# Performance work log

Hardware: AMD Instinct MI355X
Metric: run time of the kernel (lower is better)

Reference implementation:

```python
import jax, jax.numpy as jnp
import numpy as np

B, T, HID = 1, 2048, 1024
H, D = 16, 64
S = 64            # selection_block_size / sliding window / compress block
MAXK = 8          # max_selected_blocks
W_ENT, W_SP = 0.01, 0.01
NB = T // S       # 32 blocks (T divisible by S -> no padding branch)


def setup_inputs() -> dict:
    key = jax.random.key(0)
    ks = jax.random.split(key, 8)
    rn = lambda k, shp, s=0.02: jax.random.normal(k, shp, jnp.float32) * s
    return {
        'hidden_states': rn(ks[0], (B, T, HID), 1.0),
        'Wq': rn(ks[1], (HID, H * D)),
        'Wk': rn(ks[2], (HID, H * D)),
        'Wv': rn(ks[3], (HID, H * D)),
        'Wo': rn(ks[4], (H * D, HID)),
        'Wc': rn(ks[5], (S * D, D)),      # shared k/v compress MLP (same module in torch)
        'bc': jnp.zeros((D,), jnp.float32),
        'k_scale': jnp.ones((1,), jnp.float32),
        'k_bias': jnp.zeros((1,), jnp.float32),
        'Ws': rn(ks[6], (HID, 3 * H)),
        'bs': jnp.zeros((3 * H,), jnp.float32),
    }


def _local_attn(q, k, v):
    # lucidrains LocalAttention: window S, causal, look_backward=1, scale d^-0.5
    b, h, t, d = q.shape
    nw = t // S
    qw = q.reshape(b, h, nw, S, d)
    kw = k.reshape(b, h, nw, S, d)
    vw = v.reshape(b, h, nw, S, d)
    k_prev = jnp.concatenate([jnp.zeros_like(kw[:, :, :1]), kw[:, :, :-1]], axis=2)
    v_prev = jnp.concatenate([jnp.zeros_like(vw[:, :, :1]), vw[:, :, :-1]], axis=2)
    kc = jnp.concatenate([k_prev, kw], axis=3)   # (b,h,nw,2S,d)
    vc = jnp.concatenate([v_prev, vw], axis=3)
    scores = jnp.einsum('bhwid,bhwjd->bhwij', qw, kc) / jnp.sqrt(jnp.float32(d))
    qpos = jnp.arange(S)[:, None]
    krel = jnp.arange(2 * S)[None, :] - S        # key pos relative to window start
    wins = jnp.arange(nw)[:, None, None]
    allowed = (krel <= qpos)[None] & (wins * S + krel[None] >= 0)  # (nw,S,2S)
    NEG = -jnp.finfo(scores.dtype).max
    scores = jnp.where(allowed[None, None], scores, NEG)
    p = jax.nn.softmax(scores, axis=-1)
    return jnp.einsum('bhwij,bhwjd->bhwid', p, vc).reshape(b, h, t, d)


def reference(hidden_states, Wq, Wk, Wv, Wo, Wc, bc, k_scale, k_bias, Ws, bs):
    x = hidden_states
    scale = 1.0 / jnp.sqrt(jnp.float32(D))
    q = (x @ Wq).reshape(B, T, H, D).transpose(0, 2, 1, 3)
    k = (x @ Wk).reshape(B, T, H, D).transpose(0, 2, 1, 3)
    v = (x @ Wv).reshape(B, T, H, D).transpose(0, 2, 1, 3)

    sliding_out = _local_attn(q, k, v)

    # block compression (shared MLP for k and v, exact-erf GELU as in torch)
    k_blk = k.reshape(B, H, NB, S * D)
    v_blk = v.reshape(B, H, NB, S * D)
    kc = jax.nn.gelu(k_blk @ Wc + bc, approximate=False)   # (B,H,NB,D)
    vc = jax.nn.gelu(v_blk @ Wc + bc, approximate=False)

    importance = jnp.einsum('bhid,bhjd->bhij', q, kc) * scale   # (B,H,T,NB)
    comp_probs = jax.nn.softmax(importance, axis=-1)
    comp_out = jnp.einsum('bhij,bhjd->bhid', comp_probs, vc)

    # per-query-block scores, entropy-driven dynamic k
    block_scores = importance.reshape(B, H, NB, S, NB).mean(axis=3)   # (B,H,NB,NB)
    block_probs = jax.nn.softmax(block_scores, axis=-1)
    entropy = -jnp.sum(block_probs * jnp.log(block_probs + 1e-9), axis=-1)
    max_entropy = jnp.log(jnp.float32(NB))
    norm_ent = entropy / (max_entropy + 1e-9)
    k_ratio = jax.nn.sigmoid(k_scale[0] * norm_ent + k_bias[0])
    dynamic_k = jnp.clip(MAXK * k_ratio, 1.0, float(MAXK)).astype(jnp.int32)  # torch .long() truncates
    avg_k = dynamic_k.astype(jnp.float32).mean()

    _, topk_idx = jax.lax.top_k(block_scores, MAXK)                 # (B,H,NB,MAXK)
    k_mask = jnp.arange(MAXK)[None, None, None, :] < dynamic_k[..., None]
    sel = (topk_idx[..., None] == jnp.arange(NB)) & k_mask[..., None]
    mask = sel.any(axis=-2)                                         # (B,H,NB,NB)
    mask = mask | jnp.eye(NB, dtype=bool)[None, None]
    sparse_mask = jnp.repeat(jnp.repeat(mask, S, axis=2), S, axis=3)  # (B,H,T,T)

    attn = jnp.einsum('bhid,bhjd->bhij', q, k) * scale
    NEG = -jnp.finfo(attn.dtype).max
    attn = jnp.where(sparse_mask, attn, NEG)
    fine_probs = jax.nn.softmax(attn, axis=-1)
    fine_out = jnp.einsum('bhij,bhjd->bhid', fine_probs, v)

    strategy = jax.nn.sigmoid(x @ Ws + bs).reshape(B, T, H, 3).transpose(0, 2, 1, 3)  # (B,H,T,3)
    combined = jnp.stack([sliding_out, comp_out, fine_out], axis=-1)  # (B,H,T,D,3)
    out = jnp.einsum('bhnds,bhns->bhnd', combined, strategy)
    merged = out.transpose(0, 2, 1, 3).reshape(B, T, H * D)
    output = merged @ Wo

    entropy_loss = jnp.mean((k_ratio - norm_ent) ** 2)
    aux_loss = W_ENT * entropy_loss + W_SP * k_ratio.mean()
    return output, avg_k, aux_loss
```

## Files before the change

kernel.cpp:

```cpp
#include <hip/hip_runtime.h>
#include <math.h>
#include <stdint.h>

typedef unsigned short u16;
typedef short v8s __attribute__((ext_vector_type(8)));
typedef float v4f __attribute__((ext_vector_type(4)));

constexpr int kT   = 2048;
constexpr int kHID = 1024;
constexpr int kH   = 16;
constexpr int kNB  = 32;
constexpr size_t MB = 1ull << 20;

__device__ __forceinline__ float b2f(u16 u) { unsigned x = ((unsigned)u) << 16; return __uint_as_float(x); }
__device__ __forceinline__ u16 f2b(float f) {
  unsigned x = __float_as_uint(f);
  x += 0x7FFFu + ((x >> 16) & 1u);
  return (u16)(x >> 16);
}
__device__ __forceinline__ v4f mfma16(v8s a, v8s b, v4f c) {
  return __builtin_amdgcn_mfma_f32_16x16x32_bf16(a, b, c, 0, 0, 0);
}
__device__ __forceinline__ void gl_lds16(const void* g, void* l) {
  __builtin_amdgcn_global_load_lds((const __attribute__((address_space(1))) uint32_t*)g,
                                   (__attribute__((address_space(3))) uint32_t*)l, 16, 0, 0);
}

__global__ __launch_bounds__(256) void prep_kernel(
    const float* __restrict__ x, const float* __restrict__ Wq, const float* __restrict__ Wk,
    const float* __restrict__ Wv, const float* __restrict__ Wo, const float* __restrict__ Wc,
    const float* __restrict__ Wsp,
    u16* __restrict__ xh,
    u16* __restrict__ WqtH, u16* __restrict__ WktH,
    u16* __restrict__ WvtH, u16* __restrict__ WotH, u16* __restrict__ WctH, u16* __restrict__ WctL,
    u16* __restrict__ Wst) {
  __shared__ float tbuf[32][33];
  int bid = blockIdx.x;
  const int tid = threadIdx.x;
  if (bid < 1024) {
    int i = bid * 2048 + tid * 8;
    float4 a = *(const float4*)(x + i), b = *(const float4*)(x + i + 4);
    float tv[8] = {a.x, a.y, a.z, a.w, b.x, b.y, b.z, b.w};
    union { u16 s[8]; uint4 u; } hs;
#pragma unroll
    for (int e = 0; e < 8; ++e) hs.s[e] = f2b(tv[e]);
    *(uint4*)(xh + i) = hs.u;
    return;
  }
  bid -= 1024;
  const float* W; u16* Hh; u16* Ll; int Kd, Nd, bx, by;
  if (bid < 4096) {
    int wsel = bid >> 10, sub = bid & 1023;
    W  = wsel == 0 ? Wq : wsel == 1 ? Wk : wsel == 2 ? Wv : Wo;
    Hh = wsel == 0 ? WqtH : wsel == 1 ? WktH : wsel == 2 ? WvtH : WotH;
    Ll = nullptr;
    Kd = 1024; Nd = 1024;
    bx = (sub & 31) * 32; by = (sub >> 5) * 32;
  } else if (bid < 4096 + 256) {
    int sub = bid - 4096;
    W = Wc; Hh = WctH; Ll = WctL;
    Kd = 4096; Nd = 64;
    bx = (sub & 1) * 32; by = (sub >> 1) * 32;
  } else {
    int i = (bid - 4096 - 256) * 256 + tid;
    int n = i >> 10, k2 = i & 1023;
    float v = (n < 48) ? Wsp[(size_t)k2 * 48 + n] : 0.f;
    Wst[(size_t)n * 1024 + k2] = f2b(v);
    return;
  }
  const int lx = tid & 31, ly = tid >> 5;
  for (int i2 = ly; i2 < 32; i2 += 8) tbuf[i2][lx] = W[(size_t)(by + i2) * Nd + bx + lx];
  __syncthreads();
  for (int i2 = ly; i2 < 32; i2 += 8) {
    float xv = tbuf[lx][i2];
    size_t idx = (size_t)(bx + i2) * Kd + by + lx;
    u16 h = f2b(xv);
    Hh[idx] = h;
    if (Ll) Ll[idx] = f2b(xv - b2f(h));
  }
}

__global__ __launch_bounds__(256) void proj_gemm(const u16* __restrict__ xh,
                                                 const u16* __restrict__ WkH, const u16* __restrict__ WqH,
                                                 const u16* __restrict__ WvH, const u16* __restrict__ Wst,
                                                 const float* __restrict__ bsp,
                                                 u16* __restrict__ kbf, u16* __restrict__ qh,
                                                 u16* __restrict__ vbf, float* __restrict__ strat) {
  __shared__ u16 AsH[64 * 64], BsH[128 * 64];
  const int b = blockIdx.x;
  const int slot = (b & 7) * 100 + (b >> 3);
  const int panel = slot >> 5, bmi = slot & 31;
  int z, bni;
  if (panel < 8)       { z = 0; bni = panel; }
  else if (panel < 16) { z = 1; bni = panel - 8; }
  else if (panel < 24) { z = 2; bni = panel - 16; }
  else                 { z = 3; bni = 0; }
  const int bm = bmi * 64, bn = bni * 128;
  const u16* Bh = (z == 0) ? WkH : (z == 1) ? WqH : (z == 2) ? WvH : Wst;
  const int tid = threadIdx.x, w = tid >> 6, lane = tid & 63;
  const int lg = lane >> 4, l16 = lane & 15;
  const int wr = w >> 1, wc = w & 1;
  v4f acc[2][4] = {};
  for (int k0 = 0; k0 < kHID; k0 += 64) {
    __syncthreads();
#pragma unroll
    for (int p = 0; p < 2; ++p) {
      int s = tid + p * 256, row = s >> 3, sf = (s & 7) ^ (row & 7);
      gl_lds16(xh + (size_t)(bm + row) * kHID + k0 + sf * 8, (char*)AsH + s * 16);
    }
#pragma unroll
    for (int p = 0; p < 4; ++p) {
      int s = tid + p * 256, row = s >> 3, sf = (s & 7) ^ (row & 7);
      gl_lds16(Bh + (size_t)(bn + row) * kHID + k0 + sf * 8, (char*)BsH + s * 16);
    }
    __syncthreads();
#pragma unroll
    for (int kk = 0; kk < 2; ++kk) {
      v8s bh4[4];
#pragma unroll
      for (int j = 0; j < 4; ++j) {
        int col = wc * 64 + j * 16 + l16;
        bh4[j] = *(const v8s*)((const char*)BsH + col * 128 + (((kk * 4 + lg) ^ (col & 7)) * 16));
      }
#pragma unroll
      for (int i = 0; i < 2; ++i) {
        int row = wr * 32 + i * 16 + l16;
        v8s ah = *(const v8s*)((const char*)AsH + row * 128 + (((kk * 4 + lg) ^ (row & 7)) * 16));
#pragma unroll
        for (int j = 0; j < 4; ++j) acc[i][j] = mfma16(ah, bh4[j], acc[i][j]);
      }
    }
  }
#pragma unroll
  for (int i = 0; i < 2; ++i)
#pragma unroll
    for (int j = 0; j < 4; ++j)
#pragma unroll
      for (int r = 0; r < 4; ++r) {
        int row = bm + wr * 32 + i * 16 + lg * 4 + r;
        int col = bn + wc * 64 + j * 16 + l16;
        float val = acc[i][j][r];
        if (z == 3) {
          if (col < 48) strat[(size_t)row * 48 + col] = 1.f / (1.f + expf(-(val + bsp[col])));
        } else {
          u16 hh = f2b(val);
          size_t idx = (size_t)row * kHID + col;
          if (z == 0) kbf[idx] = hh;
          else if (z == 1) qh[idx] = hh;
          else vbf[idx] = hh;
        }
      }
}

__global__ __launch_bounds__(256) void cgemm_fused(const u16* __restrict__ kbf,
                                                   const u16* __restrict__ vbf,
                                                   const u16* __restrict__ WcH, const u16* __restrict__ WcL,
                                                   float* __restrict__ Pk, float* __restrict__ Pv) {
  __shared__ u16 AsH[64 * 64], BsH[64 * 64], BsL[64 * 64];
  const int bm = blockIdx.y * 64;
  const int isK = (blockIdx.z < 8);
  const int ks = isK ? blockIdx.z : blockIdx.z - 8;
  const u16* Asrc = isK ? kbf : vbf;
  float* P = isK ? Pk : Pv;
  const int tid = threadIdx.x;
  const int w = tid >> 6, lane = tid & 63;
  const int lg = lane >> 4, l16 = lane & 15;
  const int wr = w >> 1, wc = w & 1;
  v4f acc[2][2] = {};
  for (int k0 = ks * 512; k0 < ks * 512 + 512; k0 += 64) {
    __syncthreads();
#pragma unroll
    for (int ss = 0; ss < 2; ++ss) {
      int s = tid + ss * 256, row = s >> 3, sf = (s & 7) ^ (row & 7);
      int r = bm + row;
      size_t abase = ((size_t)((r & 31) * 64 + (k0 >> 6))) * kHID + (r >> 5) * 64 + sf * 8;
      gl_lds16(Asrc + abase, (char*)AsH + s * 16);
      gl_lds16(WcH + (size_t)row * 4096 + k0 + sf * 8, (char*)BsH + s * 16);
      if (isK) gl_lds16(WcL + (size_t)row * 4096 + k0 + sf * 8, (char*)BsL + s * 16);
    }
    __syncthreads();
    v8s ah[2][2], bh[2][2];
#pragma unroll
    for (int i = 0; i < 2; ++i)
#pragma unroll
      for (int kk = 0; kk < 2; ++kk) {
        int row = wr * 32 + i * 16 + l16;
        ah[i][kk] = *(const v8s*)((const char*)AsH + row * 128 + (((kk * 4 + lg) ^ (row & 7)) * 16));
        int col = wc * 32 + i * 16 + l16;
        bh[i][kk] = *(const v8s*)((const char*)BsH + col * 128 + (((kk * 4 + lg) ^ (col & 7)) * 16));
      }
#pragma unroll
    for (int i = 0; i < 2; ++i)
#pragma unroll
      for (int j = 0; j < 2; ++j) {
        acc[i][j] = mfma16(ah[i][0], bh[j][0], acc[i][j]);
        acc[i][j] = mfma16(ah[i][1], bh[j][1], acc[i][j]);
      }
    if (isK) {
      v8s bl[2][2];
#pragma unroll
      for (int i = 0; i < 2; ++i)
#pragma unroll
        for (int kk = 0; kk < 2; ++kk) {
          int col = wc * 32 + i * 16 + l16;
          bl[i][kk] = *(const v8s*)((const char*)BsL + col * 128 + (((kk * 4 + lg) ^ (col & 7)) * 16));
        }
#pragma unroll
      for (int i = 0; i < 2; ++i)
#pragma unroll
        for (int j = 0; j < 2; ++j) {
          acc[i][j] = mfma16(ah[i][0], bl[j][0], acc[i][j]);
          acc[i][j] = mfma16(ah[i][1], bl[j][1], acc[i][j]);
        }
    }
  }
#pragma unroll
  for (int i = 0; i < 2; ++i)
#pragma unroll
    for (int j = 0; j < 2; ++j)
#pragma unroll
      for (int r = 0; r < 4; ++r) {
        int row = bm + wr * 32 + i * 16 + lg * 4 + r;
        int col = wc * 32 + j * 16 + l16;
        P[(size_t)ks * 32768 + (size_t)row * 64 + col] = acc[i][j][r];
      }
}

__global__ __launch_bounds__(256) void creduce_kernel(const float* __restrict__ Pk,
                                                      const float* __restrict__ Pv,
                                                      const float* __restrict__ bc,
                                                      u16* __restrict__ kch, u16* __restrict__ kcl,
                                                      u16* __restrict__ vct) {
  int idx = blockIdx.x * 256 + threadIdx.x;
  int which = idx >> 15;
  int e = idx & 32767;
  const float* P = which ? Pv : Pk;
  float s = 0.f;
#pragma unroll
  for (int ks = 0; ks < 8; ++ks) s += P[(size_t)ks * 32768 + e];
  s += bc[e & 63];
  float g = 0.5f * s * (1.f + erff(s * 0.70710678118654752f));
  if (!which) {
    u16 hh = f2b(g);
    kch[e] = hh;
    kcl[e] = f2b(g - b2f(hh));
  } else {
    int h2 = e >> 11, j = (e >> 6) & 31, d = e & 63;
    vct[(size_t)h2 * 2048 + d * 32 + j] = f2b(g);
  }
}

__global__ __launch_bounds__(256) void impsel_mfma(const u16* __restrict__ qh,
                                                   const u16* __restrict__ kch,
                                                   const u16* __restrict__ kcl,
                                                   const u16* __restrict__ vct,
                                                   const float* __restrict__ strat,
                                                   const float* __restrict__ kscale_p,
                                                   const float* __restrict__ kbias_p,
                                                   unsigned* __restrict__ maskb,
                                                   float* __restrict__ krb,
                                                   float* __restrict__ neb,
                                                   int* __restrict__ dkb,
                                                   u16* __restrict__ merged) {
  __shared__ u16 Pl[4][16 * 32];
  __shared__ float red[4][32];
  const int tt = blockIdx.x, h = blockIdx.y;
  const int tid = threadIdx.x, w = tid >> 6, lane = tid & 63;
  const int lg = lane >> 4, l16 = lane & 15;
  const size_t qoff = (size_t)(tt * 64 + w * 16 + l16) * kHID + h * 64;
  v8s ah[2];
  ah[0] = *(const v8s*)(qh + qoff + lg * 8);
  ah[1] = *(const v8s*)(qh + qoff + 32 + lg * 8);
  v4f sa[2] = {};
#pragma unroll
  for (int ct = 0; ct < 2; ++ct) {
    int col = ct * 16 + l16;
#pragma unroll
    for (int kk = 0; kk < 2; ++kk) {
      v8s bh = *(const v8s*)(kch + ((size_t)h * 32 + col) * 64 + kk * 32 + lg * 8);
      v8s bl = *(const v8s*)(kcl + ((size_t)h * 32 + col) * 64 + kk * 32 + lg * 8);
      sa[ct] = mfma16(ah[kk], bh, sa[ct]);
      sa[ct] = mfma16(ah[kk], bl, sa[ct]);
    }
  }
#pragma unroll
  for (int ct = 0; ct < 2; ++ct)
#pragma unroll
    for (int j = 0; j < 4; ++j) sa[ct][j] *= 0.125f;
#pragma unroll
  for (int ct = 0; ct < 2; ++ct) {
    float v = sa[ct][0] + sa[ct][1] + sa[ct][2] + sa[ct][3];
    v += __shfl_xor(v, 16, 64);
    v += __shfl_xor(v, 32, 64);
    if (lg == 0) red[w][ct * 16 + l16] = v;
  }
  float linv[4];
#pragma unroll
  for (int j = 0; j < 4; ++j) {
    float m = fmaxf(sa[0][j], sa[1][j]);
#pragma unroll
    for (int mm = 1; mm < 16; mm <<= 1) m = fmaxf(m, __shfl_xor(m, mm, 64));
    float e0 = __expf(sa[0][j] - m), e1 = __expf(sa[1][j] - m);
    float s = e0 + e1;
#pragma unroll
    for (int mm = 1; mm < 16; mm <<= 1) s += __shfl_xor(s, mm, 64);
    linv[j] = 1.f / s;
    int row = lg * 4 + j;
    Pl[w][row * 32 + l16] = f2b(e0);
    Pl[w][row * 32 + 16 + l16] = f2b(e1);
  }
  v8s pa = *(const v8s*)(&Pl[w][l16 * 32 + lg * 8]);
  v4f o[4] = {};
#pragma unroll
  for (int dt = 0; dt < 4; ++dt) {
    v8s b = *(const v8s*)(vct + ((size_t)h * 64 + dt * 16 + l16) * 32 + lg * 8);
    o[dt] = mfma16(pa, b, o[dt]);
  }
#pragma unroll
  for (int dt = 0; dt < 4; ++dt)
#pragma unroll
    for (int j = 0; j < 4; ++j) {
      int t = tt * 64 + w * 16 + lg * 4 + j;
      int d = dt * 16 + l16;
      size_t mi = (size_t)t * kHID + h * 64 + d;
      merged[mi] = f2b(strat[t * 48 + h * 3 + 1] * (o[dt][j] * linv[j]));
    }
  __syncthreads();
  if (w == 0) {
    const int j = lane & 31;
    float bsj = (red[0][j] + red[1][j] + red[2][j] + red[3][j]) * (1.f / 64.f);
    float mx = bsj;
#pragma unroll
    for (int m = 1; m < 32; m <<= 1) mx = fmaxf(mx, __shfl_xor(mx, m, 64));
    float e = expf(bsj - mx);
    float lsum = e;
#pragma unroll
    for (int m = 1; m < 32; m <<= 1) lsum += __shfl_xor(lsum, m, 64);
    float p = e / lsum;
    float ent = p * logf(p + 1e-9f);
#pragma unroll
    for (int m = 1; m < 32; m <<= 1) ent += __shfl_xor(ent, m, 64);
    ent = -ent;
    float ne = ent / (logf(32.f) + 1e-9f);
    float kr = 1.f / (1.f + expf(-(kscale_p[0] * ne + kbias_p[0])));
    int dk = (int)fminf(fmaxf(8.f * kr, 1.f), 8.f);
    unsigned mword = 1u << tt;
    int taken = 0;
    for (int r = 0; r < dk; ++r) {
      float v2 = taken ? -3.4e38f : bsj;
      int idx2 = j;
#pragma unroll
      for (int m = 1; m < 32; m <<= 1) {
        float ov = __shfl_xor(v2, m, 64);
        int oi = __shfl_xor(idx2, m, 64);
        if (ov > v2 || (ov == v2 && oi < idx2)) { v2 = ov; idx2 = oi; }
      }
      mword |= (1u << idx2);
      if (j == idx2) taken = 1;
    }
    if (lane == 0) {
      maskb[h * kNB + tt] = mword;
      krb[h * kNB + tt] = kr;
      neb[h * kNB + tt] = ne;
      dkb[h * kNB + tt] = dk;
    }
  }
}

__global__ void finalize_kernel(const int* __restrict__ dkb, const float* __restrict__ krb,
                                const float* __restrict__ neb, float* __restrict__ out) {
  __shared__ float s1[512], s2[512], s3[512];
  int t2 = threadIdx.x;
  float fdk = (float)dkb[t2], kr = krb[t2], ne = neb[t2];
  float d = kr - ne;
  s1[t2] = fdk; s2[t2] = d * d; s3[t2] = kr;
  __syncthreads();
  for (int st = 256; st > 0; st >>= 1) {
    if (t2 < st) { s1[t2] += s1[t2 + st]; s2[t2] += s2[t2 + st]; s3[t2] += s3[t2 + st]; }
    __syncthreads();
  }
  if (t2 == 0) {
    out[(size_t)kT * kHID + 0] = s1[0] * (1.f / 512.f);
    out[(size_t)kT * kHID + 1] = 0.01f * (s2[0] * (1.f / 512.f)) + 0.01f * (s3[0] * (1.f / 512.f));
  }
}

__global__ __launch_bounds__(256) void fineslide_mfma(const u16* __restrict__ qh,
                                                      const u16* __restrict__ kb_,
                                                      const u16* __restrict__ vb_,
                                                      const float* __restrict__ strat,
                                                      const unsigned* __restrict__ maskb,
                                                      u16* __restrict__ merged) {
  __shared__ u16 Kb[2][64 * 64];
  __shared__ u16 Vt[2][64 * 64];
  __shared__ u16 Pl[4][16 * 64];
  const int b = blockIdx.x;
  const int xcd = b & 7, slot = b >> 3;
  const int h = xcd + 8 * (slot >> 5);
  const int qb = slot & 31;
  const unsigned mword = maskb[h * kNB + qb];
  unsigned uni = mword | (1u << qb);
  if (qb > 0) uni |= 1u << (qb - 1);
  const int tid = threadIdx.x, w = tid >> 6, lane = tid & 63;
  const int lg = lane >> 4, l16 = lane & 15;
  v8s aq[2];
  {
    const u16* qrow = qh + (size_t)(qb * 64 + w * 16 + l16) * kHID + h * 64;
    aq[0] = *(const v8s*)(qrow + lg * 8);
    aq[1] = *(const v8s*)(qrow + 32 + lg * 8);
  }
  float mF[4], lF[4], mS[4], lS[4];
  v4f oF[4] = {}, oS[4] = {};
#pragma unroll
  for (int j = 0; j < 4; ++j) { mF[j] = -1e30f; lF[j] = 0.f; mS[j] = -1e30f; lS[j] = 0.f; }

  const int vkey = tid & 63, vd0 = (tid >> 6) * 16;

  auto k_stage = [&](int buf, int jb) {
#pragma unroll
    for (int ss = 0; ss < 2; ++ss) {
      int s = tid + ss * 256;
      int key = s >> 3, sf = (s & 7) ^ (key & 7);
      gl_lds16(kb_ + (size_t)(jb * 64 + key) * kHID + h * 64 + sf * 8, (char*)Kb[buf] + s * 16);
    }
  };
  auto v_issue = [&](int jb, uint4& c0, uint4& c1) {
    const u16* vsrc = vb_ + (size_t)(jb * 64 + vkey) * kHID + h * 64 + vd0;
    c0 = *(const uint4*)(vsrc);
    c1 = *(const uint4*)(vsrc + 8);
  };
  auto v_write = [&](int buf, uint4 c0, uint4 c1) {
    union { uint4 u[2]; u16 s[16]; } c;
    c.u[0] = c0; c.u[1] = c1;
#pragma unroll
    for (int i = 0; i < 16; ++i) {
      int d = vd0 + i;
      *((u16*)((char*)Vt[buf] + d * 128 + (((vkey >> 3) ^ (d & 7)) * 16)) + (vkey & 7)) = c.s[i];
    }
  };

  auto upd = [&](const v4f* sa, float* m_run, float* l_run, v4f* o_acc, int buf) {
    float corr[4];
#pragma unroll
    for (int j = 0; j < 4; ++j) {
      float t = fmaxf(fmaxf(sa[0][j], sa[1][j]), fmaxf(sa[2][j], sa[3][j]));
#pragma unroll
      for (int mm = 1; mm < 16; mm <<= 1) t = fmaxf(t, __shfl_xor(t, mm, 64));
      float mn = fmaxf(m_run[j], t);
      corr[j] = __expf(m_run[j] - mn);
      m_run[j] = mn;
    }
    float rs[4] = {0.f, 0.f, 0.f, 0.f};
    float pv[4][4];
#pragma unroll
    for (int ct = 0; ct < 4; ++ct)
#pragma unroll
      for (int j = 0; j < 4; ++j) {
        float e = __expf(sa[ct][j] - m_run[j]);
        pv[ct][j] = e;
        rs[j] += e;
      }
#pragma unroll
    for (int j = 0; j < 4; ++j) {
#pragma unroll
      for (int mm = 1; mm < 16; mm <<= 1) rs[j] += __shfl_xor(rs[j], mm, 64);
      l_run[j] = l_run[j] * corr[j] + rs[j];
    }
#pragma unroll
    for (int ct = 0; ct < 4; ++ct)
#pragma unroll
      for (int j = 0; j < 4; ++j) {
        int row = lg * 4 + j;
        int seg = ct * 2 + (l16 >> 3);
        *((u16*)((char*)Pl + w * 2048 + row * 128 + ((seg ^ (row & 7)) * 16)) + (l16 & 7)) = f2b(pv[ct][j]);
      }
#pragma unroll
    for (int dt = 0; dt < 4; ++dt)
#pragma unroll
      for (int j = 0; j < 4; ++j) o_acc[dt][j] *= corr[j];
#pragma unroll
    for (int dt = 0; dt < 4; ++dt) {
      int d = dt * 16 + l16;
#pragma unroll
      for (int kk = 0; kk < 2; ++kk) {
        v8s pa = *(const v8s*)((const char*)Pl + w * 2048 + l16 * 128 + (((kk * 4 + lg) ^ (l16 & 7)) * 16));
        v8s vb2 = *(const v8s*)((const char*)Vt[buf] + d * 128 + (((kk * 4 + lg) ^ (d & 7)) * 16));
        o_acc[dt] = mfma16(pa, vb2, o_acc[dt]);
      }
    }
  };

  int jb_cur = __builtin_ctz(uni);
  unsigned rem = uni & (uni - 1);
  uint4 vc0, vc1;
  v_issue(jb_cur, vc0, vc1);
  k_stage(0, jb_cur);
  v_write(0, vc0, vc1);
  int buf = 0;
  while (jb_cur >= 0) {
    int jb_next = -1;
    if (rem) { jb_next = __builtin_ctz(rem); rem &= rem - 1; }
    __syncthreads();
    if (jb_next >= 0) { v_issue(jb_next, vc0, vc1); k_stage(buf ^ 1, jb_next); }
    v4f sa[4] = {};
#pragma unroll
    for (int ct = 0; ct < 4; ++ct) {
      int key = ct * 16 + l16;
#pragma unroll
      for (int kk = 0; kk < 2; ++kk) {
        v8s bk = *(const v8s*)((const char*)Kb[buf] + key * 128 + (((kk * 4 + lg) ^ (key & 7)) * 16));
        sa[ct] = mfma16(aq[kk], bk, sa[ct]);
      }
    }
#pragma unroll
    for (int ct = 0; ct < 4; ++ct)
#pragma unroll
      for (int j = 0; j < 4; ++j) sa[ct][j] *= 0.125f;
    const bool inF = (mword >> jb_cur) & 1u;
    const bool inS = (jb_cur == qb) || (jb_cur + 1 == qb);
    if (inF) upd(sa, mF, lF, oF, buf);
    if (inS) {
      v4f sb[4];
#pragma unroll
      for (int ct = 0; ct < 4; ++ct) sb[ct] = sa[ct];
      if (jb_cur == qb) {
#pragma unroll
        for (int ct = 0; ct < 4; ++ct) {
          int key = ct * 16 + l16;
#pragma unroll
          for (int j = 0; j < 4; ++j) {
            int qp = w * 16 + lg * 4 + j;
            if (key > qp) sb[ct][j] = -1e30f;
          }
        }
      }
      upd(sb, mS, lS, oS, buf);
    }
    if (jb_next >= 0) v_write(buf ^ 1, vc0, vc1);
    jb_cur = jb_next;
    buf ^= 1;
  }
#pragma unroll
  for (int dt = 0; dt < 4; ++dt)
#pragma unroll
    for (int j = 0; j < 4; ++j) {
      int row = lg * 4 + j;
      int t = qb * 64 + w * 16 + row;
      int d = dt * 16 + l16;
      size_t idx = (size_t)t * kHID + h * 64 + d;
      float add = strat[t * 48 + h * 3 + 0] * (oS[dt][j] / lS[j]) +
                  strat[t * 48 + h * 3 + 2] * (oF[dt][j] / lF[j]);
      merged[idx] = f2b(b2f(merged[idx]) + add);
    }
}

__global__ __launch_bounds__(256) void gemm_out(const u16* __restrict__ A, const u16* __restrict__ Bt,
                                                float* __restrict__ Cf) {
  __shared__ u16 As[128 * 64], Bs[64 * 64];
  const int b = blockIdx.x;
  const int g = (b & 7) * 32 + (b >> 3);
  const int bn = (g >> 4) * 64;
  const int bm = (g & 15) * 128;
  const int tid = threadIdx.x, w = tid >> 6, lane = tid & 63;
  const int lg = lane >> 4, l16 = lane & 15;
  const int K = kHID;
  v4f acc[2][4] = {};
  for (int k0 = 0; k0 < K; k0 += 64) {
    __syncthreads();
#pragma unroll
    for (int p = 0; p < 4; ++p) {
      int s = tid + p * 256, row = s >> 3, sf = (s & 7) ^ (row & 7);
      gl_lds16(A + (size_t)(bm + row) * K + k0 + sf * 8, (char*)As + s * 16);
    }
#pragma unroll
    for (int p = 0; p < 2; ++p) {
      int s = tid + p * 256, row = s >> 3, sf = (s & 7) ^ (row & 7);
      gl_lds16(Bt + (size_t)(bn + row) * K + k0 + sf * 8, (char*)Bs + s * 16);
    }
    __syncthreads();
    v8s a[2][2], bfr[4][2];
#pragma unroll
    for (int i = 0; i < 2; ++i)
#pragma unroll
      for (int kk = 0; kk < 2; ++kk) {
        int row = w * 32 + i * 16 + l16;
        a[i][kk] = *(const v8s*)((const char*)As + row * 128 + (((kk * 4 + lg) ^ (row & 7)) * 16));
      }
#pragma unroll
    for (int j = 0; j < 4; ++j)
#pragma unroll
      for (int kk = 0; kk < 2; ++kk) {
        int col = j * 16 + l16;
        bfr[j][kk] = *(const v8s*)((const char*)Bs + col * 128 + (((kk * 4 + lg) ^ (col & 7)) * 16));
      }
#pragma unroll
    for (int i = 0; i < 2; ++i)
#pragma unroll
      for (int j = 0; j < 4; ++j) {
        acc[i][j] = mfma16(a[i][0], bfr[j][0], acc[i][j]);
        acc[i][j] = mfma16(a[i][1], bfr[j][1], acc[i][j]);
      }
  }
#pragma unroll
  for (int i = 0; i < 2; ++i)
#pragma unroll
    for (int j = 0; j < 4; ++j)
#pragma unroll
      for (int r = 0; r < 4; ++r) {
        int row = bm + w * 32 + i * 16 + lg * 4 + r;
        int col = bn + j * 16 + l16;
        Cf[(size_t)row * kHID + col] = acc[i][j][r];
      }
}

extern "C" void kernel_launch(void* const* d_in, const int* in_sizes, int n_in,
                              void* d_out, int out_size, void* d_ws, size_t ws_size,
                              hipStream_t stream) {
  const float* x      = (const float*)d_in[0];
  const float* Wq     = (const float*)d_in[1];
  const float* Wk     = (const float*)d_in[2];
  const float* Wv     = (const float*)d_in[3];
  const float* Wo     = (const float*)d_in[4];
  const float* Wc     = (const float*)d_in[5];
  const float* bc     = (const float*)d_in[6];
  const float* kscale = (const float*)d_in[7];
  const float* kbias  = (const float*)d_in[8];
  const float* Wsp    = (const float*)d_in[9];
  const float* bsp    = (const float*)d_in[10];
  float* out = (float*)d_out;
  char* W = (char*)d_ws;

  u16* qh     = (u16*)(W + 0 * MB);
  u16* kbf    = (u16*)(W + 8 * MB);
  u16* vbf    = (u16*)(W + 16 * MB);
  u16* merged = (u16*)(W + 20 * MB);
  u16* xh     = (u16*)(W + 24 * MB);
  u16* WqtH   = (u16*)(W + 32 * MB);
  u16* WktH   = (u16*)(W + 36 * MB);
  u16* WvtH   = (u16*)(W + 40 * MB);
  u16* WotH   = (u16*)(W + 42 * MB);
  u16* WctH   = (u16*)(W + 44 * MB);
  u16* WctL   = (u16*)(W + 44 * MB + 512 * 1024);
  u16* Wst    = (u16*)(W + 45 * MB);
  float* strat= (float*)(W + 46 * MB);
  float* Pk   = (float*)(W + 47 * MB);
  float* Pv   = (float*)(W + 48 * MB);
  u16* kchb   = (u16*)(W + 49 * MB);
  u16* kclb   = (u16*)(W + 49 * MB + 64 * 1024);
  u16* vctb   = (u16*)(W + 49 * MB + 128 * 1024);
  unsigned* maskb = (unsigned*)(W + 49 * MB + 192 * 1024);
  float* krb  = (float*)(W + 49 * MB + 196 * 1024);
  float* neb  = (float*)(W + 49 * MB + 200 * 1024);
  int*   dkb  = (int*)(W + 49 * MB + 204 * 1024);

  dim3 b256(256);
  prep_kernel<<<5888, b256, 0, stream>>>(x, Wq, Wk, Wv, Wo, Wc, Wsp,
                                         xh, WqtH, WktH, WvtH, WotH, WctH, WctL, Wst);
  proj_gemm<<<800, b256, 0, stream>>>(xh, WktH, WqtH, WvtH, Wst,
                                      bsp, kbf, qh, vbf, strat);
  cgemm_fused<<<dim3(1, 8, 16), b256, 0, stream>>>(kbf, vbf, WctH, WctL, Pk, Pv);
  creduce_kernel<<<256, b256, 0, stream>>>(Pk, Pv, bc, kchb, kclb, vctb);
  impsel_mfma<<<dim3(32, kH), b256, 0, stream>>>(qh, kchb, kclb, vctb, strat,
                                                 kscale, kbias, maskb, krb, neb, dkb, merged);
  finalize_kernel<<<1, 512, 0, stream>>>(dkb, krb, neb, out);
  fineslide_mfma<<<512, b256, 0, stream>>>(qh, kbf, vbf, strat, maskb, merged);
  gemm_out<<<256, b256, 0, stream>>>(merged, WotH, out);
}
```

Baseline: 96.20 us.

## Fuse compress reduction into impsel, fold finalize into fineslide, retile output GEMM

The split-K reduction, bias and GELU of the compress MLP move into impsel_mfma, so every block rebuilds its head's compressed K (hi/lo bf16) and transposed V in swizzled LDS. This drops the creduce kernel and its workspace round trip. The finalize reduction now runs in one wavefront of fineslide block 0, removing another launch. gemm_out moves from 128x64 to 64x64 tiles with 512 blocks to fill more CUs. In exchange, the compress reduction is recomputed 32 times per head, and the smaller GEMM tiles get less operand reuse.

```diff
diff --git a/kernel.cpp b/kernel.cpp
--- a/kernel.cpp
+++ b/kernel.cpp
@@ -226,34 +226,10 @@
       }
 }
 
-__global__ __launch_bounds__(256) void creduce_kernel(const float* __restrict__ Pk,
-                                                      const float* __restrict__ Pv,
-                                                      const float* __restrict__ bc,
-                                                      u16* __restrict__ kch, u16* __restrict__ kcl,
-                                                      u16* __restrict__ vct) {
-  int idx = blockIdx.x * 256 + threadIdx.x;
-  int which = idx >> 15;
-  int e = idx & 32767;
-  const float* P = which ? Pv : Pk;
-  float s = 0.f;
-#pragma unroll
-  for (int ks = 0; ks < 8; ++ks) s += P[(size_t)ks * 32768 + e];
-  s += bc[e & 63];
-  float g = 0.5f * s * (1.f + erff(s * 0.70710678118654752f));
-  if (!which) {
-    u16 hh = f2b(g);
-    kch[e] = hh;
-    kcl[e] = f2b(g - b2f(hh));
-  } else {
-    int h2 = e >> 11, j = (e >> 6) & 31, d = e & 63;
-    vct[(size_t)h2 * 2048 + d * 32 + j] = f2b(g);
-  }
-}
-
 __global__ __launch_bounds__(256) void impsel_mfma(const u16* __restrict__ qh,
-                                                   const u16* __restrict__ kch,
-                                                   const u16* __restrict__ kcl,
-                                                   const u16* __restrict__ vct,
+                                                   const float* __restrict__ Pk,
+                                                   const float* __restrict__ Pv,
+                                                   const float* __restrict__ bc,
                                                    const float* __restrict__ strat,
                                                    const float* __restrict__ kscale_p,
                                                    const float* __restrict__ kbias_p,
@@ -262,11 +238,56 @@
                                                    float* __restrict__ neb,
                                                    int* __restrict__ dkb,
                                                    u16* __restrict__ merged) {
+  __shared__ u16 KCH[32 * 64], KCL[32 * 64], VCT[64 * 32];
   __shared__ u16 Pl[4][16 * 32];
   __shared__ float red[4][32];
   const int tt = blockIdx.x, h = blockIdx.y;
   const int tid = threadIdx.x, w = tid >> 6, lane = tid & 63;
   const int lg = lane >> 4, l16 = lane & 15;
+  {
+    int nb = tid >> 3, seg = tid & 7;
+    {
+      const float* base = Pk + ((size_t)(h * 32 + nb) * 64 + seg * 8);
+      float v[8] = {};
+#pragma unroll
+      for (int ks = 0; ks < 8; ++ks) {
+        const float* p = base + (size_t)ks * 32768;
+        float4 a = *(const float4*)p, bq = *(const float4*)(p + 4);
+        v[0] += a.x; v[1] += a.y; v[2] += a.z; v[3] += a.w;
+        v[4] += bq.x; v[5] += bq.y; v[6] += bq.z; v[7] += bq.w;
+      }
+      v8s hi, lo;
+#pragma unroll
+      for (int e = 0; e < 8; ++e) {
+        float s = v[e] + bc[seg * 8 + e];
+        float g = 0.5f * s * (1.f + erff(s * 0.70710678118654752f));
+        u16 hh = f2b(g);
+        hi[e] = (short)hh;
+        lo[e] = (short)f2b(g - b2f(hh));
+      }
+      *(v8s*)((char*)KCH + nb * 128 + ((seg ^ (nb & 7)) * 16)) = hi;
+      *(v8s*)((char*)KCL + nb * 128 + ((seg ^ (nb & 7)) * 16)) = lo;
+    }
+    {
+      const float* base = Pv + ((size_t)(h * 32 + nb) * 64 + seg * 8);
+      float v[8] = {};
+#pragma unroll
+      for (int ks = 0; ks < 8; ++ks) {
+        const float* p = base + (size_t)ks * 32768;
+        float4 a = *(const float4*)p, bq = *(const float4*)(p + 4);
+        v[0] += a.x; v[1] += a.y; v[2] += a.z; v[3] += a.w;
+        v[4] += bq.x; v[5] += bq.y; v[6] += bq.z; v[7] += bq.w;
+      }
+#pragma unroll
+      for (int e = 0; e < 8; ++e) {
+        int d = seg * 8 + e;
+        float s = v[e] + bc[d];
+        float g = 0.5f * s * (1.f + erff(s * 0.70710678118654752f));
+        *((u16*)((char*)VCT + d * 64 + (((nb >> 3) ^ (d & 3)) * 16) + (nb & 7) * 2)) = f2b(g);
+      }
+    }
+  }
+  __syncthreads();
   const size_t qoff = (size_t)(tt * 64 + w * 16 + l16) * kHID + h * 64;
   v8s ah[2];
   ah[0] = *(const v8s*)(qh + qoff + lg * 8);
@@ -277,8 +298,9 @@
     int col = ct * 16 + l16;
 #pragma unroll
     for (int kk = 0; kk < 2; ++kk) {
-      v8s bh = *(const v8s*)(kch + ((size_t)h * 32 + col) * 64 + kk * 32 + lg * 8);
-      v8s bl = *(const v8s*)(kcl + ((size_t)h * 32 + col) * 64 + kk * 32 + lg * 8);
+      int bo = col * 128 + (((kk * 4 + lg) ^ (col & 7)) * 16);
+      v8s bh = *(const v8s*)((const char*)KCH + bo);
+      v8s bl = *(const v8s*)((const char*)KCL + bo);
       sa[ct] = mfma16(ah[kk], bh, sa[ct]);
       sa[ct] = mfma16(ah[kk], bl, sa[ct]);
     }
@@ -313,7 +335,8 @@
   v4f o[4] = {};
 #pragma unroll
   for (int dt = 0; dt < 4; ++dt) {
-    v8s b = *(const v8s*)(vct + ((size_t)h * 64 + dt * 16 + l16) * 32 + lg * 8);
+    int d = dt * 16 + l16;
+    v8s b = *(const v8s*)((const char*)VCT + d * 64 + ((lg ^ (d & 3)) * 16));
     o[dt] = mfma16(pa, b, o[dt]);
   }
 #pragma unroll
@@ -367,29 +390,15 @@
   }
 }
 
-__global__ void finalize_kernel(const int* __restrict__ dkb, const float* __restrict__ krb,
-                                const float* __restrict__ neb, float* __restrict__ out) {
-  __shared__ float s1[512], s2[512], s3[512];
-  int t2 = threadIdx.x;
-  float fdk = (float)dkb[t2], kr = krb[t2], ne = neb[t2];
-  float d = kr - ne;
-  s1[t2] = fdk; s2[t2] = d * d; s3[t2] = kr;
-  __syncthreads();
-  for (int st = 256; st > 0; st >>= 1) {
-    if (t2 < st) { s1[t2] += s1[t2 + st]; s2[t2] += s2[t2 + st]; s3[t2] += s3[t2 + st]; }
-    __syncthreads();
-  }
-  if (t2 == 0) {
-    out[(size_t)kT * kHID + 0] = s1[0] * (1.f / 512.f);
-    out[(size_t)kT * kHID + 1] = 0.01f * (s2[0] * (1.f / 512.f)) + 0.01f * (s3[0] * (1.f / 512.f));
-  }
-}
-
 __global__ __launch_bounds__(256) void fineslide_mfma(const u16* __restrict__ qh,
                                                       const u16* __restrict__ kb_,
                                                       const u16* __restrict__ vb_,
                                                       const float* __restrict__ strat,
                                                       const unsigned* __restrict__ maskb,
+                                                      const float* __restrict__ krb,
+                                                      const float* __restrict__ neb,
+                                                      const int* __restrict__ dkb,
+                                                      float* __restrict__ outp,
                                                       u16* __restrict__ merged) {
   __shared__ u16 Kb[2][64 * 64];
   __shared__ u16 Vt[2][64 * 64];
@@ -403,6 +412,24 @@
   if (qb > 0) uni |= 1u << (qb - 1);
   const int tid = threadIdx.x, w = tid >> 6, lane = tid & 63;
   const int lg = lane >> 4, l16 = lane & 15;
+  if (b == 0 && w == 0) {
+    float s1 = 0.f, s2 = 0.f, s3 = 0.f;
+    for (int i = lane; i < 512; i += 64) {
+      float fdk = (float)dkb[i], kr = krb[i], ne = neb[i];
+      float d2 = kr - ne;
+      s1 += fdk; s2 += d2 * d2; s3 += kr;
+    }
+#pragma unroll
+    for (int m = 1; m < 64; m <<= 1) {
+      s1 += __shfl_xor(s1, m, 64);
+      s2 += __shfl_xor(s2, m, 64);
+      s3 += __shfl_xor(s3, m, 64);
+    }
+    if (lane == 0) {
+      outp[(size_t)kT * kHID + 0] = s1 * (1.f / 512.f);
+      outp[(size_t)kT * kHID + 1] = 0.01f * (s2 * (1.f / 512.f)) + 0.01f * (s3 * (1.f / 512.f));
+    }
+  }
   v8s aq[2];
   {
     const u16* qrow = qh + (size_t)(qb * 64 + w * 16 + l16) * kHID + h * 64;
@@ -556,61 +583,43 @@
 
 __global__ __launch_bounds__(256) void gemm_out(const u16* __restrict__ A, const u16* __restrict__ Bt,
                                                 float* __restrict__ Cf) {
-  __shared__ u16 As[128 * 64], Bs[64 * 64];
+  __shared__ u16 As[64 * 64], Bs[64 * 64];
   const int b = blockIdx.x;
-  const int g = (b & 7) * 32 + (b >> 3);
-  const int bn = (g >> 4) * 64;
-  const int bm = (g & 15) * 128;
+  const int g = (b & 7) * 64 + (b >> 3);
+  const int bn = (g >> 5) * 64;
+  const int bm = (g & 31) * 64;
   const int tid = threadIdx.x, w = tid >> 6, lane = tid & 63;
   const int lg = lane >> 4, l16 = lane & 15;
-  const int K = kHID;
-  v4f acc[2][4] = {};
-  for (int k0 = 0; k0 < K; k0 += 64) {
+  v4f acc[4] = {};
+  for (int k0 = 0; k0 < kHID; k0 += 64) {
     __syncthreads();
-#pragma unroll
-    for (int p = 0; p < 4; ++p) {
-      int s = tid + p * 256, row = s >> 3, sf = (s & 7) ^ (row & 7);
-      gl_lds16(A + (size_t)(bm + row) * K + k0 + sf * 8, (char*)As + s * 16);
-    }
 #pragma unroll
     for (int p = 0; p < 2; ++p) {
       int s = tid + p * 256, row = s >> 3, sf = (s & 7) ^ (row & 7);
-      gl_lds16(Bt + (size_t)(bn + row) * K + k0 + sf * 8, (char*)Bs + s * 16);
+      gl_lds16(A + (size_t)(bm + row) * kHID + k0 + sf * 8, (char*)As + s * 16);
+      gl_lds16(Bt + (size_t)(bn + row) * kHID + k0 + sf * 8, (char*)Bs + s * 16);
     }
     __syncthreads();
-    v8s a[2][2], bfr[4][2];
-#pragma unroll
-    for (int i = 0; i < 2; ++i)
-#pragma unroll
-      for (int kk = 0; kk < 2; ++kk) {
-        int row = w * 32 + i * 16 + l16;
-        a[i][kk] = *(const v8s*)((const char*)As + row * 128 + (((kk * 4 + lg) ^ (row & 7)) * 16));
-      }
-#pragma unroll
-    for (int j = 0; j < 4; ++j)
-#pragma unroll
-      for (int kk = 0; kk < 2; ++kk) {
+#pragma unroll
+    for (int kk = 0; kk < 2; ++kk) {
+      int row = w * 16 + l16;
+      v8s a = *(const v8s*)((const char*)As + row * 128 + (((kk * 4 + lg) ^ (row & 7)) * 16));
+#pragma unroll
+      for (int j = 0; j < 4; ++j) {
         int col = j * 16 + l16;
-        bfr[j][kk] = *(const v8s*)((const char*)Bs + col * 128 + (((kk * 4 + lg) ^ (col & 7)) * 16));
-      }
-#pragma unroll
-    for (int i = 0; i < 2; ++i)
-#pragma unroll
-      for (int j = 0; j < 4; ++j) {
-        acc[i][j] = mfma16(a[i][0], bfr[j][0], acc[i][j]);
-        acc[i][j] = mfma16(a[i][1], bfr[j][1], acc[i][j]);
-      }
-  }
-#pragma unroll
-  for (int i = 0; i < 2; ++i)
-#pragma unroll
-    for (int j = 0; j < 4; ++j)
-#pragma unroll
-      for (int r = 0; r < 4; ++r) {
-        int row = bm + w * 32 + i * 16 + lg * 4 + r;
-        int col = bn + j * 16 + l16;
-        Cf[(size_t)row * kHID + col] = acc[i][j][r];
-      }
+        v8s bb = *(const v8s*)((const char*)Bs + col * 128 + (((kk * 4 + lg) ^ (col & 7)) * 16));
+        acc[j] = mfma16(a, bb, acc[j]);
+      }
+    }
+  }
+#pragma unroll
+  for (int j = 0; j < 4; ++j)
+#pragma unroll
+    for (int r = 0; r < 4; ++r) {
+      int row = bm + w * 16 + lg * 4 + r;
+      int col = bn + j * 16 + l16;
+      Cf[(size_t)row * kHID + col] = acc[j][r];
+    }
 }
 
 extern "C" void kernel_launch(void* const* d_in, const int* in_sizes, int n_in,
@@ -645,13 +654,10 @@
   float* strat= (float*)(W + 46 * MB);
   float* Pk   = (float*)(W + 47 * MB);
   float* Pv   = (float*)(W + 48 * MB);
-  u16* kchb   = (u16*)(W + 49 * MB);
-  u16* kclb   = (u16*)(W + 49 * MB + 64 * 1024);
-  u16* vctb   = (u16*)(W + 49 * MB + 128 * 1024);
-  unsigned* maskb = (unsigned*)(W + 49 * MB + 192 * 1024);
-  float* krb  = (float*)(W + 49 * MB + 196 * 1024);
-  float* neb  = (float*)(W + 49 * MB + 200 * 1024);
-  int*   dkb  = (int*)(W + 49 * MB + 204 * 1024);
+  unsigned* maskb = (unsigned*)(W + 49 * MB);
+  float* krb  = (float*)(W + 49 * MB + 4 * 1024);
+  float* neb  = (float*)(W + 49 * MB + 8 * 1024);
+  int*   dkb  = (int*)(W + 49 * MB + 12 * 1024);
 
   dim3 b256(256);
   prep_kernel<<<5888, b256, 0, stream>>>(x, Wq, Wk, Wv, Wo, Wc, Wsp,
@@ -659,10 +665,9 @@
   proj_gemm<<<800, b256, 0, stream>>>(xh, WktH, WqtH, WvtH, Wst,
                                       bsp, kbf, qh, vbf, strat);
   cgemm_fused<<<dim3(1, 8, 16), b256, 0, stream>>>(kbf, vbf, WctH, WctL, Pk, Pv);
-  creduce_kernel<<<256, b256, 0, stream>>>(Pk, Pv, bc, kchb, kclb, vctb);
-  impsel_mfma<<<dim3(32, kH), b256, 0, stream>>>(qh, kchb, kclb, vctb, strat,
+  impsel_mfma<<<dim3(32, kH), b256, 0, stream>>>(qh, Pk, Pv, bc, strat,
                                                  kscale, kbias, maskb, krb, neb, dkb, merged);
-  finalize_kernel<<<1, 512, 0, stream>>>(dkb, krb, neb, out);
-  fineslide_mfma<<<512, b256, 0, stream>>>(qh, kbf, vbf, strat, maskb, merged);
-  gemm_out<<<256, b256, 0, stream>>>(merged, WotH, out);
-}
+  fineslide_mfma<<<512, b256, 0, stream>>>(qh, kbf, vbf, strat, maskb,
+                                           krb, neb, dkb, out, merged);
+  gemm_out<<<512, b256, 0, stream>>>(merged, WotH, out);
+}
```

New measurement: 93.91 us. -2.4%, faster.
